# Kernel tuning notes

Hardware: AMD Instinct MI355X
Metric: run time of the kernel (lower is better)

Reference implementation:

```python
import jax, jax.numpy as jnp
import numpy as np

EMBED_DIM = 1024
NUM_HEADS = 16
HEAD_DIM = EMBED_DIM // NUM_HEADS
L, B, S = 2048, 2, 2048


def setup_inputs() -> dict:
    key = jax.random.key(0)
    kq, kk, kv = jax.random.split(key, 3)
    q = jax.random.normal(kq, (L, B, EMBED_DIM), dtype=jnp.float32)
    k = jax.random.normal(kk, (S, B, EMBED_DIM), dtype=jnp.float32)
    v = jax.random.normal(kv, (S, B, EMBED_DIM), dtype=jnp.float32)
    return {"q": q, "k": k, "v": v}


def reference(q, k, v):
    Lq, Bq, D = q.shape
    Sq = k.shape[0]
    scaling = HEAD_DIM ** -0.5
    # (L, B, D) -> (B*H, L, head_dim), matching reshape + transpose in torch
    qh = (q * scaling).reshape(Lq, Bq * NUM_HEADS, HEAD_DIM).transpose(1, 0, 2)
    kh = k.reshape(Sq, Bq * NUM_HEADS, HEAD_DIM).transpose(1, 0, 2)
    vh = v.reshape(Sq, Bq * NUM_HEADS, HEAD_DIM).transpose(1, 0, 2)
    # qk: (B*H, L, S) -- the full attention matrix the module materializes
    qk = jnp.einsum('ild,isd->ils', qh, kh)
    attn = jax.nn.softmax(qk, axis=-1)
    # dropout_p = 0.0 -> identity
    out = jnp.einsum('ils,isd->ild', attn, vh)  # (B*H, L, head_dim)
    out = out.transpose(1, 0, 2).reshape(Lq, Bq, D)
    return out
```

## Files before the change

### kernel.cpp

```cpp
#include <hip/hip_runtime.h>
#include <hip/hip_bf16.h>
#include <math.h>

typedef __bf16 bf16x8 __attribute__((ext_vector_type(8)));
typedef __bf16 bf16x4 __attribute__((ext_vector_type(4)));
typedef float  f32x4  __attribute__((ext_vector_type(4)));

constexpr int EMBED = 1024;
constexpr int NH    = 16;
constexpr int HD    = 64;
constexpr int LL    = 2048;
constexpr int BB    = 2;
constexpr int SSEQ  = 2048;

constexpr int BQ = 64;
constexpr int BK = 64;
constexpr int NT = SSEQ / BK;

constexpr size_t KW_ELEMS = (size_t)BB * NH * SSEQ * HD;

__device__ __forceinline__ void gload16(const void* g, void* l) {
  __builtin_amdgcn_global_load_lds((const __attribute__((address_space(1))) unsigned int*)g,
                                   (__attribute__((address_space(3))) unsigned int*)l, 16, 0, 0);
}

__device__ __forceinline__ float exp2_fast(float x) {
  float r;
  asm("v_exp_f32 %0, %1" : "=v"(r) : "v"(x));
  return r;
}

__global__ __launch_bounds__(256) void prep_kv(const float* __restrict__ Kg,
                                               const float* __restrict__ Vg,
                                               __hip_bfloat16* __restrict__ kw,
                                               __hip_bfloat16* __restrict__ vtw) {
  const int bid = blockIdx.x;
  if (bid < 2048) {
    const int idx = bid * 256 + threadIdx.x;
    const int e8 = idx & 127;
    const int t2 = idx >> 7;
    const int b  = t2 & 1;
    const int s  = t2 >> 1;
    const int h  = e8 >> 3;
    const int d8 = e8 & 7;
    const float* src = Kg + ((size_t)s * BB + b) * EMBED + e8 * 8;
    float4 a = *(const float4*)src;
    float4 c = *(const float4*)(src + 4);
    bf16x8 w;
    w[0] = (__bf16)a.x; w[1] = (__bf16)a.y; w[2] = (__bf16)a.z; w[3] = (__bf16)a.w;
    w[4] = (__bf16)c.x; w[5] = (__bf16)c.y; w[6] = (__bf16)c.z; w[7] = (__bf16)c.w;
    *(bf16x8*)(kw + (((size_t)(b * NH + h) * SSEQ + s) * HD + d8 * 8)) = w;
  } else {
    const int idx = (bid - 2048) * 256 + threadIdx.x;
    const int e  = idx & 1023;
    const int t2 = idx >> 10;
    const int b  = t2 & 1;
    const int s0 = (t2 >> 1) * 8;
    const int h  = e >> 6;
    const int d  = e & 63;
    const float* src = Vg + ((size_t)s0 * BB + b) * EMBED + e;
    bf16x8 w;
#pragma unroll
    for (int i = 0; i < 8; ++i) w[i] = (__bf16)src[(size_t)i * BB * EMBED];
    *(bf16x8*)(vtw + (((size_t)(b * NH + h) * HD + d) * SSEQ + s0)) = w;
  }
}

__global__ __launch_bounds__(256) void sdpa_fwd(const float* __restrict__ Qg,
                                                const __hip_bfloat16* __restrict__ Kw,
                                                const __hip_bfloat16* __restrict__ VTw,
                                                float* __restrict__ Og) {
  __shared__ char sh[40960];
  char* kbuf = sh;
  char* vbuf = sh + 16384;
  char* psh  = sh + 32768;

  const int tid  = threadIdx.x;
  const int wv   = tid >> 6;
  const int lane = tid & 63;
  const int g    = lane >> 4;
  const int qc   = lane & 15;

  const int bh = blockIdx.y;
  const int bb = bh >> 4;
  const int hh = bh & 15;

  const size_t rstride = (size_t)BB * EMBED;
  const float* qb = Qg + (size_t)bb * EMBED + hh * HD;
  float*       ob = Og + (size_t)bb * EMBED + hh * HD;
  const char*  kwb = (const char*)(Kw + (size_t)bh * SSEQ * HD);
  const char*  vtb = (const char*)(VTw + (size_t)bh * HD * SSEQ);

  const int qrow0 = blockIdx.x * BQ + wv * 16;

  const int r0  = (wv * 2 + 0) * 8 + (lane >> 3);
  const int r1  = (wv * 2 + 1) * 8 + (lane >> 3);
  const int ch0 = (lane & 7) ^ (r0 & 7);
  const int ch1 = (lane & 7) ^ (r1 & 7);
  const char* kg0 = kwb + r0 * 128 + ch0 * 16;
  const char* kg1 = kwb + r1 * 128 + ch1 * 16;
  const char* vg0 = vtb + r0 * 4096 + ch0 * 16;
  const char* vg1 = vtb + r1 * 4096 + ch1 * 16;
  char* kd0 = kbuf + (wv * 2 + 0) * 1024;
  char* kd1 = kbuf + (wv * 2 + 1) * 1024;
  char* vd0 = vbuf + (wv * 2 + 0) * 1024;
  char* vd1 = vbuf + (wv * 2 + 1) * 1024;

#define STAGE(B, T)                                        \
  do {                                                     \
    gload16(kg0 + (size_t)(T) * 8192, kd0 + (B) * 8192);   \
    gload16(kg1 + (size_t)(T) * 8192, kd1 + (B) * 8192);   \
    gload16(vg0 + (size_t)(T) * 128,  vd0 + (B) * 8192);   \
    gload16(vg1 + (size_t)(T) * 128,  vd1 + (B) * 8192);   \
  } while (0)

  constexpr float QSC = 0.125f * 1.4426950408889634f;
  bf16x8 qf[2];
  {
    const float* qr = qb + (size_t)(qrow0 + qc) * rstride;
#pragma unroll
    for (int f = 0; f < 2; ++f) {
      const float* p = qr + f * 32 + g * 8;
      float4 a = *(const float4*)p;
      float4 c = *(const float4*)(p + 4);
      qf[f][0] = (__bf16)(a.x * QSC); qf[f][1] = (__bf16)(a.y * QSC);
      qf[f][2] = (__bf16)(a.z * QSC); qf[f][3] = (__bf16)(a.w * QSC);
      qf[f][4] = (__bf16)(c.x * QSC); qf[f][5] = (__bf16)(c.y * QSC);
      qf[f][6] = (__bf16)(c.z * QSC); qf[f][7] = (__bf16)(c.w * QSC);
    }
  }

  f32x4 acc[4];
#pragma unroll
  for (int nb = 0; nb < 4; ++nb) { acc[nb][0] = 0.f; acc[nb][1] = 0.f; acc[nb][2] = 0.f; acc[nb][3] = 0.f; }
  float m = -INFINITY;
  float l = 0.f;

  STAGE(0, 0);
  __syncthreads();
  int cur = 0;

  for (int t = 0; t < NT; ++t) {
    if (t + 1 < NT) STAGE(cur ^ 1, t + 1);

    const char* kb = kbuf + cur * 8192;
    const char* vb = vbuf + cur * 8192;
    const int sw = (qc & 7) << 4;

    f32x4 st[4];
#pragma unroll
    for (int sb = 0; sb < 4; ++sb) {
      const int base = (sb * 16 + qc) * 128;
      bf16x8 k0 = *(const bf16x8*)(kb + base + ((g * 16)      ^ sw));
      bf16x8 k1 = *(const bf16x8*)(kb + base + ((64 + g * 16) ^ sw));
      f32x4 a; a[0] = 0.f; a[1] = 0.f; a[2] = 0.f; a[3] = 0.f;
      a = __builtin_amdgcn_mfma_f32_16x16x32_bf16(k0, qf[0], a, 0, 0, 0);
      a = __builtin_amdgcn_mfma_f32_16x16x32_bf16(k1, qf[1], a, 0, 0, 0);
      st[sb] = a;
    }

    float mx = st[0][0];
#pragma unroll
    for (int sb = 0; sb < 4; ++sb)
#pragma unroll
      for (int r2 = 0; r2 < 4; ++r2) mx = fmaxf(mx, st[sb][r2]);
    mx = fmaxf(mx, __shfl_xor(mx, 16));
    mx = fmaxf(mx, __shfl_xor(mx, 32));
    const float mnew  = fmaxf(m, mx);
    const float alpha = exp2_fast(m - mnew);
    m = mnew;
    float rs = 0.f;
#pragma unroll
    for (int sb = 0; sb < 4; ++sb)
#pragma unroll
      for (int r2 = 0; r2 < 4; ++r2) {
        float p = exp2_fast(st[sb][r2] - mnew);
        st[sb][r2] = p;
        rs += p;
      }
    rs += __shfl_xor(rs, 16);
    rs += __shfl_xor(rs, 32);
    l = l * alpha + rs;

    float ar[4];
#pragma unroll
    for (int r2 = 0; r2 < 4; ++r2) ar[r2] = __shfl(alpha, g * 4 + r2);
#pragma unroll
    for (int nb = 0; nb < 4; ++nb)
#pragma unroll
      for (int r2 = 0; r2 < 4; ++r2) acc[nb][r2] *= ar[r2];

    {
      char* pw = psh + wv * 2048;
#pragma unroll
      for (int sb = 0; sb < 4; ++sb) {
        bf16x4 p4;
        p4[0] = (__bf16)st[sb][0]; p4[1] = (__bf16)st[sb][1];
        p4[2] = (__bf16)st[sb][2]; p4[3] = (__bf16)st[sb][3];
        *(bf16x4*)(pw + qc * 128 + ((sb * 32 + g * 8) ^ sw)) = p4;
      }
      asm volatile("s_waitcnt lgkmcnt(0)" ::: "memory");
    }

    {
      const char* pw = psh + wv * 2048;
      bf16x8 pa0 = *(const bf16x8*)(pw + qc * 128 + ((g * 16)      ^ sw));
      bf16x8 pa1 = *(const bf16x8*)(pw + qc * 128 + ((64 + g * 16) ^ sw));
#pragma unroll
      for (int nb = 0; nb < 4; ++nb) {
        const int vbase = (nb * 16 + qc) * 128;
        bf16x8 v0f = *(const bf16x8*)(vb + vbase + ((g * 16)      ^ sw));
        bf16x8 v1f = *(const bf16x8*)(vb + vbase + ((64 + g * 16) ^ sw));
        acc[nb] = __builtin_amdgcn_mfma_f32_16x16x32_bf16(pa0, v0f, acc[nb], 0, 0, 0);
        acc[nb] = __builtin_amdgcn_mfma_f32_16x16x32_bf16(pa1, v1f, acc[nb], 0, 0, 0);
      }
    }

    __syncthreads();
    cur ^= 1;
  }
#undef STAGE

  float linv[4];
#pragma unroll
  for (int r2 = 0; r2 < 4; ++r2) {
    float lr = __shfl(l, g * 4 + r2);
    linv[r2] = 1.0f / lr;
  }
#pragma unroll
  for (int nb = 0; nb < 4; ++nb)
#pragma unroll
    for (int r2 = 0; r2 < 4; ++r2) {
      const int row = qrow0 + g * 4 + r2;
      ob[(size_t)row * rstride + nb * 16 + qc] = acc[nb][r2] * linv[r2];
    }
}

extern "C" void kernel_launch(void* const* d_in, const int* in_sizes, int n_in,
                              void* d_out, int out_size, void* d_ws, size_t ws_size,
                              hipStream_t stream) {
  const float* q = (const float*)d_in[0];
  const float* k = (const float*)d_in[1];
  const float* v = (const float*)d_in[2];
  float* o = (float*)d_out;
  __hip_bfloat16* kw  = (__hip_bfloat16*)d_ws;
  __hip_bfloat16* vtw = kw + KW_ELEMS;

  prep_kv<<<dim3(4096), dim3(256), 0, stream>>>(k, v, kw, vtw);
  dim3 grid(LL / BQ, BB * NH);
  sdpa_fwd<<<grid, dim3(256), 0, stream>>>(q, kw, vtw, o);
}
```

Before: 158.3 us.

## Transpose V through LDS in prep, add lazy softmax rescale and MFMA priority

The V transpose in the prep kernel now goes through a swizzled LDS tile. Each block reads coalesced 64x64 tiles and writes contiguous transposed rows, replacing strided scalar global loads, and the grid drops to 3072 blocks. The attention loop skips the running-max rescale of the accumulator when no row's max has grown by more than 8 (in log2 units), which removes shuffles and multiplies on most iterations at the cost of p values that can reach up to 2^8. It also raises wave priority around the MFMA sections so matrix work issues ahead of other waves.

New measurement: 154.5 us. -2.4%, faster.

```diff
diff --git a/kernel.cpp b/kernel.cpp
--- a/kernel.cpp
+++ b/kernel.cpp
@@ -34,6 +34,7 @@
                                                const float* __restrict__ Vg,
                                                __hip_bfloat16* __restrict__ kw,
                                                __hip_bfloat16* __restrict__ vtw) {
+  __shared__ char tsh[64 * 128];
   const int bid = blockIdx.x;
   if (bid < 2048) {
     const int idx = bid * 256 + threadIdx.x;
@@ -51,18 +52,50 @@
     w[4] = (__bf16)c.x; w[5] = (__bf16)c.y; w[6] = (__bf16)c.z; w[7] = (__bf16)c.w;
     *(bf16x8*)(kw + (((size_t)(b * NH + h) * SSEQ + s) * HD + d8 * 8)) = w;
   } else {
-    const int idx = (bid - 2048) * 256 + threadIdx.x;
-    const int e  = idx & 1023;
-    const int t2 = idx >> 10;
-    const int b  = t2 & 1;
-    const int s0 = (t2 >> 1) * 8;
-    const int h  = e >> 6;
-    const int d  = e & 63;
-    const float* src = Vg + ((size_t)s0 * BB + b) * EMBED + e;
-    bf16x8 w;
-#pragma unroll
-    for (int i = 0; i < 8; ++i) w[i] = (__bf16)src[(size_t)i * BB * EMBED];
-    *(bf16x8*)(vtw + (((size_t)(b * NH + h) * HD + d) * SSEQ + s0)) = w;
+    const int vb2 = bid - 2048;
+    const int st  = vb2 & 31;
+    const int bh  = vb2 >> 5;
+    const int b   = bh >> 4;
+    const int h   = bh & 15;
+    const int t   = threadIdx.x;
+
+    {
+      const int r  = t >> 2;
+      const int c0 = (t & 3) * 16;
+      const float* src = Vg + ((size_t)(st * 64 + r) * BB + b) * EMBED + h * HD + c0;
+      float4 x0 = *(const float4*)(src);
+      float4 x1 = *(const float4*)(src + 4);
+      float4 x2 = *(const float4*)(src + 8);
+      float4 x3 = *(const float4*)(src + 12);
+      bf16x8 w0, w1;
+      w0[0] = (__bf16)x0.x; w0[1] = (__bf16)x0.y; w0[2] = (__bf16)x0.z; w0[3] = (__bf16)x0.w;
+      w0[4] = (__bf16)x1.x; w0[5] = (__bf16)x1.y; w0[6] = (__bf16)x1.z; w0[7] = (__bf16)x1.w;
+      w1[0] = (__bf16)x2.x; w1[1] = (__bf16)x2.y; w1[2] = (__bf16)x2.z; w1[3] = (__bf16)x2.w;
+      w1[4] = (__bf16)x3.x; w1[5] = (__bf16)x3.y; w1[6] = (__bf16)x3.z; w1[7] = (__bf16)x3.w;
+      const int colb = ((c0 + (r >> 3) * 16) & 63) * 2;
+      char* rowp = tsh + r * 128;
+      *(bf16x8*)(rowp + colb)      = w0;
+      *(bf16x8*)(rowp + colb + 16) = w1;
+    }
+    __syncthreads();
+    {
+      const int d   = t >> 2;
+      const int sc0 = (t & 3) * 16;
+      bf16x8 o0, o1;
+#pragma unroll
+      for (int i = 0; i < 8; ++i) {
+        const int s = sc0 + i;
+        o0[i] = *(const __bf16*)(tsh + s * 128 + (((d + (s >> 3) * 16) & 63) * 2));
+      }
+#pragma unroll
+      for (int i = 8; i < 16; ++i) {
+        const int s = sc0 + i;
+        o1[i - 8] = *(const __bf16*)(tsh + s * 128 + (((d + (s >> 3) * 16) & 63) * 2));
+      }
+      __hip_bfloat16* dst = vtw + ((size_t)(bh * HD + d)) * SSEQ + st * 64 + sc0;
+      *(bf16x8*)(dst)     = o0;
+      *(bf16x8*)(dst + 8) = o1;
+    }
   }
 }
 
@@ -148,6 +181,7 @@
     const int sw = (qc & 7) << 4;
 
     f32x4 st[4];
+    __builtin_amdgcn_s_setprio(1);
 #pragma unroll
     for (int sb = 0; sb < 4; ++sb) {
       const int base = (sb * 16 + qc) * 128;
@@ -158,37 +192,45 @@
       a = __builtin_amdgcn_mfma_f32_16x16x32_bf16(k1, qf[1], a, 0, 0, 0);
       st[sb] = a;
     }
-
-    float mx = st[0][0];
-#pragma unroll
-    for (int sb = 0; sb < 4; ++sb)
-#pragma unroll
-      for (int r2 = 0; r2 < 4; ++r2) mx = fmaxf(mx, st[sb][r2]);
+    __builtin_amdgcn_s_setprio(0);
+
+    float mx;
+    {
+      float m0 = fmaxf(fmaxf(st[0][0], st[0][1]), fmaxf(st[0][2], st[0][3]));
+      float m1 = fmaxf(fmaxf(st[1][0], st[1][1]), fmaxf(st[1][2], st[1][3]));
+      float m2 = fmaxf(fmaxf(st[2][0], st[2][1]), fmaxf(st[2][2], st[2][3]));
+      float m3 = fmaxf(fmaxf(st[3][0], st[3][1]), fmaxf(st[3][2], st[3][3]));
+      mx = fmaxf(fmaxf(m0, m1), fmaxf(m2, m3));
+    }
     mx = fmaxf(mx, __shfl_xor(mx, 16));
     mx = fmaxf(mx, __shfl_xor(mx, 32));
-    const float mnew  = fmaxf(m, mx);
-    const float alpha = exp2_fast(m - mnew);
-    m = mnew;
+
+    if (!__all(mx - m <= 8.0f)) {
+      const float mnew  = fmaxf(m, mx);
+      const float alpha = exp2_fast(m - mnew);
+      m = mnew;
+      l *= alpha;
+      float ar[4];
+#pragma unroll
+      for (int r2 = 0; r2 < 4; ++r2) ar[r2] = __shfl(alpha, g * 4 + r2);
+#pragma unroll
+      for (int nb = 0; nb < 4; ++nb)
+#pragma unroll
+        for (int r2 = 0; r2 < 4; ++r2) acc[nb][r2] *= ar[r2];
+    }
+
     float rs = 0.f;
 #pragma unroll
     for (int sb = 0; sb < 4; ++sb)
 #pragma unroll
       for (int r2 = 0; r2 < 4; ++r2) {
-        float p = exp2_fast(st[sb][r2] - mnew);
+        float p = exp2_fast(st[sb][r2] - m);
         st[sb][r2] = p;
         rs += p;
       }
     rs += __shfl_xor(rs, 16);
     rs += __shfl_xor(rs, 32);
-    l = l * alpha + rs;
-
-    float ar[4];
-#pragma unroll
-    for (int r2 = 0; r2 < 4; ++r2) ar[r2] = __shfl(alpha, g * 4 + r2);
-#pragma unroll
-    for (int nb = 0; nb < 4; ++nb)
-#pragma unroll
-      for (int r2 = 0; r2 < 4; ++r2) acc[nb][r2] *= ar[r2];
+    l += rs;
 
     {
       char* pw = psh + wv * 2048;
@@ -206,6 +248,7 @@
       const char* pw = psh + wv * 2048;
       bf16x8 pa0 = *(const bf16x8*)(pw + qc * 128 + ((g * 16)      ^ sw));
       bf16x8 pa1 = *(const bf16x8*)(pw + qc * 128 + ((64 + g * 16) ^ sw));
+      __builtin_amdgcn_s_setprio(1);
 #pragma unroll
       for (int nb = 0; nb < 4; ++nb) {
         const int vbase = (nb * 16 + qc) * 128;
@@ -214,6 +257,7 @@
         acc[nb] = __builtin_amdgcn_mfma_f32_16x16x32_bf16(pa0, v0f, acc[nb], 0, 0, 0);
         acc[nb] = __builtin_amdgcn_mfma_f32_16x16x32_bf16(pa1, v1f, acc[nb], 0, 0, 0);
       }
+      __builtin_amdgcn_s_setprio(0);
     }
 
     __syncthreads();
@@ -246,7 +290,7 @@
   __hip_bfloat16* kw  = (__hip_bfloat16*)d_ws;
   __hip_bfloat16* vtw = kw + KW_ELEMS;
 
-  prep_kv<<<dim3(4096), dim3(256), 0, stream>>>(k, v, kw, vtw);
+  prep_kv<<<dim3(3072), dim3(256), 0, stream>>>(k, v, kw, vtw);
   dim3 grid(LL / BQ, BB * NH);
   sdpa_fwd<<<grid, dim3(256), 0, stream>>>(q, kw, vtw, o);
 }
```
